# Kernel tuning notes

Measured on AMD Instinct MI355X. Metric: run time of the kernel, lower is better.

Reference implementation:

```python
import jax, jax.numpy as jnp
import numpy as np

MAX_DEG = 3
DEG_DIMS = [1, 3, 5, 7]          # degree_to_dim(d) = 2d+1
SUM_DIM = 16                     # sum of DEG_DIMS
FREQ_SUM = 44                    # sum over (d_in,d_out) of 2*min(d_in,d_out)+1
C = 32                           # channels per degree (in == out, FULL fusion)
EDGE_DIM = 2                     # fiber_edge[0] + 1
MID = 32                         # RadialProfile mid_dim
E = 4096
N = 1024


def setup_inputs() -> dict:
    key = jax.random.key(0)
    ks = jax.random.split(key, 16)
    inp = {}
    for d, dim in enumerate(DEG_DIMS):
        inp[f"node_feats_{d}"] = jax.random.normal(ks[d], (N, C, dim), jnp.float32)
    inp["edge_feats_0"] = jax.random.normal(ks[4], (E, EDGE_DIM, 1), jnp.float32)
    inp["basis"] = jax.random.normal(ks[5], (E, SUM_DIM, FREQ_SUM, SUM_DIM), jnp.float32)
    inp["src"] = jax.random.randint(ks[6], (E,), 0, N, dtype=jnp.int32)
    inp["dst"] = jax.random.randint(ks[7], (E,), 0, N, dtype=jnp.int32)
    # RadialProfile params: Linear(2,32) -> ReLU -> Linear(32,32) -> ReLU -> Linear(32, 44*32*32, bias=False)
    inp["w1"] = jax.random.normal(ks[8], (EDGE_DIM, MID), jnp.float32) / np.sqrt(EDGE_DIM)
    inp["b1"] = jnp.zeros((MID,), jnp.float32)
    inp["w2"] = jax.random.normal(ks[9], (MID, MID), jnp.float32) / np.sqrt(MID)
    inp["b2"] = jnp.zeros((MID,), jnp.float32)
    inp["w3"] = jax.random.normal(ks[10], (MID, FREQ_SUM * C * C), jnp.float32) / np.sqrt(MID)
    # self-interaction kernels per output degree
    for d in range(MAX_DEG + 1):
        inp[f"kernel_self_{d}"] = jax.random.normal(ks[11 + d], (C, C), jnp.float32) / np.sqrt(C)
    return inp


def _conv_se3(node_feats, edge_feats_0, basis, src, dst,
              w1, b1, w2, b2, w3, kernels_self):
    e = edge_feats_0.shape[0]
    # invariant edge feats: [E, edge_dim]
    inv = edge_feats_0[..., 0]
    # gather source node features and fuse along representation dim: [E, C, 16]
    feats = jnp.concatenate([nf[src] for nf in node_feats], axis=-1)
    # RadialProfile MLP -> radial weights [E, C_out, C_in * FREQ_SUM]
    h = jax.nn.relu(inv @ w1 + b1)
    h = jax.nn.relu(h @ w2 + b2)
    radial_weights = (h @ w3).reshape(e, C, C * FREQ_SUM)
    # VersatileConvSE3 fused path:
    # tmp = (features @ basis_view).view(E, C*FREQ_SUM, SUM_DIM)
    basis_view = basis.reshape(e, SUM_DIM, FREQ_SUM * SUM_DIM)
    tmp = jnp.einsum('eci,eix->ecx', feats, basis_view).reshape(e, C * FREQ_SUM, SUM_DIM)
    out_fused = jnp.einsum('eok,eks->eos', radial_weights, tmp)  # [E, C, 16]
    # unfuse by degree, add self-interaction at dst, pool (copy_e_sum) to nodes
    outs = []
    off = 0
    for d, dim in enumerate(DEG_DIMS):
        o = out_fused[..., off:off + dim]
        o = o + jnp.einsum('oc,ecd->eod', kernels_self[d], node_feats[d][dst])
        outs.append(jax.ops.segment_sum(o, dst, num_segments=N))
        off += dim
    # return fused node output [N, C, 16] (concat of degrees 0..3)
    return jnp.concatenate(outs, axis=-1)


def reference(node_feats_0, node_feats_1, node_feats_2, node_feats_3,
              edge_feats_0, basis, src, dst,
              w1, b1, w2, b2, w3,
              kernel_self_0, kernel_self_1, kernel_self_2, kernel_self_3):
    return _conv_se3([node_feats_0, node_feats_1, node_feats_2, node_feats_3],
                     edge_feats_0, basis, src, dst,
                     w1, b1, w2, b2, w3,
                     [kernel_self_0, kernel_self_1, kernel_self_2, kernel_self_3])
```

## Files before the change

kernel.cpp:

```cpp
#include <hip/hip_runtime.h>
#include <hip/hip_bf16.h>

#define NN 1024
#define EE 4096
#define CC 32
#define SD 16
#define FQ 44
#define MIDC 32
#define EB 16
#define NFQ 4
#define FPB 11

typedef short s16x4 __attribute__((ext_vector_type(4)));
typedef short s16x8 __attribute__((ext_vector_type(8)));
typedef float fx4 __attribute__((ext_vector_type(4)));

__device__ __forceinline__ unsigned short f2b(float x) {
    __hip_bfloat16 b = __float2bfloat16(x);
    return *reinterpret_cast<unsigned short*>(&b);
}

__device__ __forceinline__ s16x4 pack4(float a, float b, float c, float d) {
    s16x4 r;
    r[0] = (short)f2b(a); r[1] = (short)f2b(b);
    r[2] = (short)f2b(c); r[3] = (short)f2b(d);
    return r;
}

__device__ __forceinline__ fx4 mfma16(s16x4 a, s16x4 b, fx4 c) {
#if defined(__HIP_DEVICE_COMPILE__)
#if __has_builtin(__builtin_amdgcn_mfma_f32_16x16x16_bf16)
    return __builtin_amdgcn_mfma_f32_16x16x16_bf16(a, b, c, 0, 0, 0);
#else
    return __builtin_amdgcn_mfma_f32_16x16x16bf16_1k(a, b, c, 0, 0, 0);
#endif
#else
    return c;
#endif
}

__global__ __launch_bounds__(256) void k_w3t2(const float* __restrict__ w3,
                                              unsigned short* __restrict__ w3t2) {
    int tid = blockIdx.x * 256 + threadIdx.x;
    int m = tid & 31;
    int o = (tid >> 5) & 31;
    int c = tid >> 10;
    const float* rp = &w3[(size_t)m * 45056 + o * 1408 + c * 44];
    float v[44];
#pragma unroll
    for (int q = 0; q < 11; q++) {
        float4 t4 = *(const float4*)(rp + q * 4);
        v[q * 4 + 0] = t4.x; v[q * 4 + 1] = t4.y;
        v[q * 4 + 2] = t4.z; v[q * 4 + 3] = t4.w;
    }
#pragma unroll
    for (int f = 0; f < FQ; f++) {
        w3t2[(((size_t)f * CC + o) * CC + c) * CC + m] = f2b(v[f]);
    }
}

__global__ __launch_bounds__(256) void k_h(const float* __restrict__ ef,
                                           const float* __restrict__ w1,
                                           const float* __restrict__ b1,
                                           const float* __restrict__ w2,
                                           const float* __restrict__ b2,
                                           const int* __restrict__ dst,
                                           unsigned short* __restrict__ h2,
                                           int* __restrict__ deg) {
    int e = blockIdx.x * 256 + threadIdx.x;
    if (e >= EE) return;
    float i0 = ef[e * 2 + 0], i1 = ef[e * 2 + 1];
    float h1[MIDC];
#pragma unroll
    for (int j = 0; j < MIDC; j++) {
        float v = i0 * w1[j] + i1 * w1[MIDC + j] + b1[j];
        h1[j] = v > 0.f ? v : 0.f;
    }
    for (int j = 0; j < MIDC; j++) {
        float v = b2[j];
#pragma unroll
        for (int m = 0; m < MIDC; m++) v += h1[m] * w2[m * MIDC + j];
        v = v > 0.f ? v : 0.f;
        h2[e * MIDC + j] = f2b(v);
    }
    atomicAdd(&deg[dst[e]], 1);
}

__global__ __launch_bounds__(512, 4) void k_main(
    const float* __restrict__ nf0, const float* __restrict__ nf1,
    const float* __restrict__ nf2, const float* __restrict__ nf3,
    const float* __restrict__ basis, const int* __restrict__ src,
    const int* __restrict__ dst, const unsigned short* __restrict__ h2,
    const unsigned short* __restrict__ w3t2, float* __restrict__ out) {
    __shared__ __align__(16) unsigned short rad_lds[EB * CC * CC];

    int t = threadIdx.x;
    int wv = t >> 6;
    int l = t & 63;
    int l15 = l & 15;
    int kg = l >> 4;
    int eg = blockIdx.x >> 2;
    int fq = blockIdx.x & 3;
    int eb = eg * EB;
    int f0 = fq * FPB;

    s16x8 h2frag = *(const s16x8*)(h2 + ((size_t)(eb + l15) * MIDC + (kg << 3)));

    s16x4 fa[2][2];
#pragma unroll
    for (int ei = 0; ei < 2; ei++) {
        int sn = src[eb + (wv << 1) + ei];
#pragma unroll
        for (int ch = 0; ch < 2; ch++) {
            int c = (ch << 4) + l15;
            s16x4 v;
#pragma unroll
            for (int j = 0; j < 4; j++) {
                int i = (kg << 2) + j;
                float x;
                if (i < 1) x = nf0[sn * CC + c];
                else if (i < 4) x = nf1[(sn * CC + c) * 3 + (i - 1)];
                else if (i < 9) x = nf2[(sn * CC + c) * 5 + (i - 4)];
                else x = nf3[(sn * CC + c) * 7 + (i - 9)];
                v[j] = (short)f2b(x);
            }
            fa[ei][ch] = v;
        }
    }

    int radw[8];
#pragma unroll
    for (int j = 0; j < 8; j++) {
        int o = (wv << 2) + (j >> 1), ch = j & 1;
        int b = (l15 << 11) | (o << 6) | (ch << 5) | (kg << 3);
        radw[j] = b ^ (((l15 ^ o) & 15) << 3);
    }
    int rada[2][2][2];
#pragma unroll
    for (int ei = 0; ei < 2; ei++) {
        int e = (wv << 1) + ei;
#pragma unroll
        for (int oh = 0; oh < 2; oh++) {
            int o = (oh << 4) + l15;
#pragma unroll
            for (int ch = 0; ch < 2; ch++) {
                int b = (e << 11) | (o << 6) | (ch << 5) | (kg << 3);
                rada[ei][oh][ch] = b ^ (((e ^ o) & 15) << 3);
            }
        }
    }

    fx4 acc[2][2];
#pragma unroll
    for (int q = 0; q < 4; q++) acc[q >> 1][q & 1] = (fx4){0.f, 0.f, 0.f, 0.f};
    fx4 zz = (fx4){0.f, 0.f, 0.f, 0.f};

    s16x8 w[8];
    float pf[2][4];

#define LOAD_W(F)                                                                       \
    {                                                                                   \
        _Pragma("unroll") for (int j = 0; j < 8; j++) {                                 \
            int o_ = (wv << 2) + (j >> 1), ch_ = j & 1;                                 \
            w[j] = *(const s16x8*)(w3t2 +                                               \
                ((((size_t)(F) * CC + o_) * CC + (ch_ << 4) + l15) * CC + (kg << 3)));  \
        }                                                                               \
    }
#define LOAD_PF(F)                                                                      \
    {                                                                                   \
        _Pragma("unroll") for (int ei_ = 0; ei_ < 2; ei_++) {                           \
            const float* bp = basis +                                                   \
                (((size_t)(eb + (wv << 1) + ei_) * SD + (kg << 2)) * FQ + (F)) * SD +   \
                l15;                                                                    \
            _Pragma("unroll") for (int j = 0; j < 4; j++)                               \
                pf[ei_][j] = bp[(size_t)j * (FQ * SD)];                                 \
        }                                                                               \
    }

    LOAD_W(f0);
    LOAD_PF(f0);

    for (int fi = 0; fi < FPB; fi++) {
        __builtin_amdgcn_s_setprio(1);
#pragma unroll
        for (int j = 0; j < 8; j++) {
            fx4 cf = __builtin_amdgcn_mfma_f32_16x16x32_bf16(w[j], h2frag, zz, 0, 0, 0);
            *(s16x4*)((char*)rad_lds + radw[j]) = pack4(cf[0], cf[1], cf[2], cf[3]);
        }
        __builtin_amdgcn_s_setprio(0);
        s16x4 bbf[2];
#pragma unroll
        for (int ei = 0; ei < 2; ei++)
            bbf[ei] = pack4(pf[ei][0], pf[ei][1], pf[ei][2], pf[ei][3]);
        if (fi + 1 < FPB) {
            int fn = f0 + fi + 1;
            LOAD_W(fn);
            LOAD_PF(fn);
        }
        __syncthreads();

        __builtin_amdgcn_s_setprio(1);
#pragma unroll
        for (int ei = 0; ei < 2; ei++) {
#pragma unroll
            for (int ch = 0; ch < 2; ch++) {
                fx4 u = mfma16(fa[ei][ch], bbf[ei], zz);
                s16x4 ub = pack4(u[0], u[1], u[2], u[3]);
#pragma unroll
                for (int oh = 0; oh < 2; oh++) {
                    s16x4 ra = *(const s16x4*)((char*)rad_lds + rada[ei][oh][ch]);
                    acc[ei][oh] = mfma16(ra, ub, acc[ei][oh]);
                }
            }
        }
        __builtin_amdgcn_s_setprio(0);
        __syncthreads();
    }

#pragma unroll
    for (int ei = 0; ei < 2; ei++) {
        int e = (wv << 1) + ei;
        int d = dst[eb + e];
        float* op = &out[(size_t)d * (CC * SD)];
#pragma unroll
        for (int oh = 0; oh < 2; oh++) {
#pragma unroll
            for (int r = 0; r < 4; r++) {
                int o = (oh << 4) + (kg << 2) + r;
                atomicAdd(&op[o * SD + l15], acc[ei][oh][r]);
            }
        }
    }
}

__global__ __launch_bounds__(256) void k_self(
    const float* __restrict__ nf0, const float* __restrict__ nf1,
    const float* __restrict__ nf2, const float* __restrict__ nf3,
    const float* __restrict__ ks0, const float* __restrict__ ks1,
    const float* __restrict__ ks2, const float* __restrict__ ks3,
    const int* __restrict__ deg, float* __restrict__ out) {
    int idx = blockIdx.x * 256 + threadIdx.x;
    if (idx >= NN * CC * SD) return;
    int n = idx >> 9;
    int rem = idx & 511;
    int o = rem >> 4;
    int s = rem & 15;
    const float* nf;
    const float* ks;
    int dim, off;
    if (s < 1) { nf = nf0; ks = ks0; dim = 1; off = 0; }
    else if (s < 4) { nf = nf1; ks = ks1; dim = 3; off = 1; }
    else if (s < 9) { nf = nf2; ks = ks2; dim = 5; off = 4; }
    else { nf = nf3; ks = ks3; dim = 7; off = 9; }
    int j = s - off;
    float acc = 0.f;
#pragma unroll
    for (int c = 0; c < CC; c++) acc += ks[o * CC + c] * nf[(n * CC + c) * dim + j];
    out[idx] += (float)deg[n] * acc;
}

extern "C" void kernel_launch(void* const* d_in, const int* in_sizes, int n_in,
                              void* d_out, int out_size, void* d_ws, size_t ws_size,
                              hipStream_t stream) {
    const float* nf0 = (const float*)d_in[0];
    const float* nf1 = (const float*)d_in[1];
    const float* nf2 = (const float*)d_in[2];
    const float* nf3 = (const float*)d_in[3];
    const float* ef = (const float*)d_in[4];
    const float* basis = (const float*)d_in[5];
    const int* src = (const int*)d_in[6];
    const int* dst = (const int*)d_in[7];
    const float* w1 = (const float*)d_in[8];
    const float* b1 = (const float*)d_in[9];
    const float* w2 = (const float*)d_in[10];
    const float* b2 = (const float*)d_in[11];
    const float* w3 = (const float*)d_in[12];
    const float* ks0 = (const float*)d_in[13];
    const float* ks1 = (const float*)d_in[14];
    const float* ks2 = (const float*)d_in[15];
    const float* ks3 = (const float*)d_in[16];
    float* out = (float*)d_out;

    unsigned short* h2 = (unsigned short*)d_ws;
    int* deg = (int*)((char*)d_ws + EE * MIDC * 2);
    unsigned short* w3t2 = (unsigned short*)((char*)d_ws + EE * MIDC * 2 + 4096);

    (void)hipMemsetAsync(d_out, 0, (size_t)out_size * sizeof(float), stream);
    (void)hipMemsetAsync(deg, 0, NN * sizeof(int), stream);

    k_w3t2<<<128, 256, 0, stream>>>(w3, w3t2);
    k_h<<<EE / 256, 256, 0, stream>>>(ef, w1, b1, w2, b2, dst, h2, deg);
    k_main<<<(EE / EB) * NFQ, 512, 0, stream>>>(nf0, nf1, nf2, nf3, basis, src, dst,
                                                h2, w3t2, out);
    k_self<<<(NN * CC * SD) / 256, 256, 0, stream>>>(nf0, nf1, nf2, nf3, ks0, ks1,
                                                     ks2, ks3, deg, out);
}
```

Before: 125.5 us.

## Double-buffer radial weights in LDS to drop one barrier per frequency step

Radial weights go into two LDS buffers. Each step computes the next frequency's weights into the other buffer while consuming the current one, so only one __syncthreads per iteration remains instead of two. Basis prefetch is now two steps ahead through ping-pong register slots, and the loop is fully unrolled. This doubles LDS use per block (from 32 KB to 64 KB), which may reduce occupancy under the 512-thread, 4-blocks launch bounds, and it raises register pressure.

```diff
diff --git a/kernel.cpp b/kernel.cpp
--- a/kernel.cpp
+++ b/kernel.cpp
@@ -92,7 +92,7 @@
     const float* __restrict__ basis, const int* __restrict__ src,
     const int* __restrict__ dst, const unsigned short* __restrict__ h2,
     const unsigned short* __restrict__ w3t2, float* __restrict__ out) {
-    __shared__ __align__(16) unsigned short rad_lds[EB * CC * CC];
+    __shared__ __align__(16) unsigned short rad_lds[2][EB * CC * CC];
 
     int t = threadIdx.x;
     int wv = t >> 6;
@@ -156,7 +156,7 @@
     fx4 zz = (fx4){0.f, 0.f, 0.f, 0.f};
 
     s16x8 w[8];
-    float pf[2][4];
+    float pfA[2][4], pfB[2][4];
 
 #define LOAD_W(F)                                                                       \
     {                                                                                   \
@@ -166,38 +166,54 @@
                 ((((size_t)(F) * CC + o_) * CC + (ch_ << 4) + l15) * CC + (kg << 3)));  \
         }                                                                               \
     }
-#define LOAD_PF(F)                                                                      \
+#define LOAD_PF(F, SLOT)                                                                \
     {                                                                                   \
         _Pragma("unroll") for (int ei_ = 0; ei_ < 2; ei_++) {                           \
             const float* bp = basis +                                                   \
                 (((size_t)(eb + (wv << 1) + ei_) * SD + (kg << 2)) * FQ + (F)) * SD +   \
                 l15;                                                                    \
             _Pragma("unroll") for (int j = 0; j < 4; j++)                               \
-                pf[ei_][j] = bp[(size_t)j * (FQ * SD)];                                 \
+                SLOT[ei_][j] = bp[(size_t)j * (FQ * SD)];                               \
         }                                                                               \
     }
-
+#define RAD(BUF)                                                                        \
+    {                                                                                   \
+        __builtin_amdgcn_s_setprio(1);                                                  \
+        _Pragma("unroll") for (int j = 0; j < 8; j++) {                                 \
+            fx4 cf = __builtin_amdgcn_mfma_f32_16x16x32_bf16(w[j], h2frag, zz, 0, 0, 0);\
+            *(s16x4*)((char*)rad_lds[BUF] + radw[j]) = pack4(cf[0], cf[1], cf[2], cf[3]);\
+        }                                                                               \
+        __builtin_amdgcn_s_setprio(0);                                                  \
+    }
+
+    LOAD_PF(f0, pfA);
     LOAD_W(f0);
-    LOAD_PF(f0);
-
+    RAD(0);
+    s16x4 bbf[2];
+    bbf[0] = pack4(pfA[0][0], pfA[0][1], pfA[0][2], pfA[0][3]);
+    bbf[1] = pack4(pfA[1][0], pfA[1][1], pfA[1][2], pfA[1][3]);
+    LOAD_PF(f0 + 1, pfA);
+    LOAD_W(f0 + 1);
+    __syncthreads();
+
+#pragma unroll
     for (int fi = 0; fi < FPB; fi++) {
-        __builtin_amdgcn_s_setprio(1);
-#pragma unroll
-        for (int j = 0; j < 8; j++) {
-            fx4 cf = __builtin_amdgcn_mfma_f32_16x16x32_bf16(w[j], h2frag, zz, 0, 0, 0);
-            *(s16x4*)((char*)rad_lds + radw[j]) = pack4(cf[0], cf[1], cf[2], cf[3]);
-        }
-        __builtin_amdgcn_s_setprio(0);
-        s16x4 bbf[2];
-#pragma unroll
-        for (int ei = 0; ei < 2; ei++)
-            bbf[ei] = pack4(pf[ei][0], pf[ei][1], pf[ei][2], pf[ei][3]);
-        if (fi + 1 < FPB) {
-            int fn = f0 + fi + 1;
-            LOAD_W(fn);
-            LOAD_PF(fn);
-        }
-        __syncthreads();
+        int f = f0 + fi;
+        int cur = fi & 1;
+        if (fi + 2 < FPB) {
+            if (cur == 0) { LOAD_PF(f + 2, pfB); }
+            else          { LOAD_PF(f + 2, pfA); }
+        }
+        if (fi + 1 < FPB) RAD(cur ^ 1);
+        s16x4 bbf_next[2];
+        if (cur == 0) {
+            bbf_next[0] = pack4(pfA[0][0], pfA[0][1], pfA[0][2], pfA[0][3]);
+            bbf_next[1] = pack4(pfA[1][0], pfA[1][1], pfA[1][2], pfA[1][3]);
+        } else {
+            bbf_next[0] = pack4(pfB[0][0], pfB[0][1], pfB[0][2], pfB[0][3]);
+            bbf_next[1] = pack4(pfB[1][0], pfB[1][1], pfB[1][2], pfB[1][3]);
+        }
+        if (fi + 2 < FPB) LOAD_W(f + 2);
 
         __builtin_amdgcn_s_setprio(1);
 #pragma unroll
@@ -208,12 +224,14 @@
                 s16x4 ub = pack4(u[0], u[1], u[2], u[3]);
 #pragma unroll
                 for (int oh = 0; oh < 2; oh++) {
-                    s16x4 ra = *(const s16x4*)((char*)rad_lds + rada[ei][oh][ch]);
+                    s16x4 ra = *(const s16x4*)((char*)rad_lds[cur] + rada[ei][oh][ch]);
                     acc[ei][oh] = mfma16(ra, ub, acc[ei][oh]);
                 }
             }
         }
         __builtin_amdgcn_s_setprio(0);
+        bbf[0] = bbf_next[0];
+        bbf[1] = bbf_next[1];
         __syncthreads();
     }
 
```

New measurement: 122.4 us. 2.5% less time.

## Process 64 edges per block to reuse radial weights and restructure pipeline

Applied to the files above, without the earlier changes.

Each block now handles 64 edges instead of 16. Every loaded w3t2 fragment is multiplied against four h2 fragments, so global and L2 traffic for radial weights per edge falls. Basis prefetch is moved ahead of the radial MFMAs and the w3 prefetch after them. A custom waitcnt+barrier replaces __syncthreads, and the trailing barrier on the last iteration is skipped. The trade-off is a 128KB LDS buffer and much larger register arrays, which limit the kernel to one block per CU and sharply cut latency hiding. The grid also shrinks to 256 blocks.

```diff
diff --git a/kernel.cpp b/kernel.cpp
--- a/kernel.cpp
+++ b/kernel.cpp
@@ -7,7 +7,7 @@
 #define SD 16
 #define FQ 44
 #define MIDC 32
-#define EB 16
+#define EB 64
 #define NFQ 4
 #define FPB 11
 
@@ -38,6 +38,9 @@
     return c;
 #endif
 }
+
+#define CBAR() asm volatile("s_waitcnt lgkmcnt(0)\n\ts_barrier" ::: "memory")
+#define MEMFENCE() asm volatile("" ::: "memory")
 
 __global__ __launch_bounds__(256) void k_w3t2(const float* __restrict__ w3,
                                               unsigned short* __restrict__ w3t2) {
@@ -86,7 +89,7 @@
     atomicAdd(&deg[dst[e]], 1);
 }
 
-__global__ __launch_bounds__(512, 4) void k_main(
+__global__ __launch_bounds__(512, 2) void k_main(
     const float* __restrict__ nf0, const float* __restrict__ nf1,
     const float* __restrict__ nf2, const float* __restrict__ nf3,
     const float* __restrict__ basis, const int* __restrict__ src,
@@ -96,20 +99,22 @@
 
     int t = threadIdx.x;
     int wv = t >> 6;
-    int l = t & 63;
-    int l15 = l & 15;
-    int kg = l >> 4;
-    int eg = blockIdx.x >> 2;
-    int fq = blockIdx.x & 3;
+    int l15 = t & 15;
+    int kg = (t >> 4) & 3;
+    int fq = blockIdx.x >> 6;
+    int eg = blockIdx.x & 63;
     int eb = eg * EB;
     int f0 = fq * FPB;
 
-    s16x8 h2frag = *(const s16x8*)(h2 + ((size_t)(eb + l15) * MIDC + (kg << 3)));
-
-    s16x4 fa[2][2];
-#pragma unroll
-    for (int ei = 0; ei < 2; ei++) {
-        int sn = src[eb + (wv << 1) + ei];
+    s16x8 h2f[4];
+#pragma unroll
+    for (int es = 0; es < 4; es++)
+        h2f[es] = *(const s16x8*)(h2 + ((size_t)(eb + (es << 4) + l15) * MIDC + (kg << 3)));
+
+    s16x4 fa[8][2];
+#pragma unroll
+    for (int u = 0; u < 8; u++) {
+        int sn = src[eb + (wv << 3) + u];
 #pragma unroll
         for (int ch = 0; ch < 2; ch++) {
             int c = (ch << 4) + l15;
@@ -124,7 +129,7 @@
                 else x = nf3[(sn * CC + c) * 7 + (i - 9)];
                 v[j] = (short)f2b(x);
             }
-            fa[ei][ch] = v;
+            fa[u][ch] = v;
         }
     }
 
@@ -135,28 +140,20 @@
         int b = (l15 << 11) | (o << 6) | (ch << 5) | (kg << 3);
         radw[j] = b ^ (((l15 ^ o) & 15) << 3);
     }
-    int rada[2][2][2];
-#pragma unroll
-    for (int ei = 0; ei < 2; ei++) {
-        int e = (wv << 1) + ei;
-#pragma unroll
-        for (int oh = 0; oh < 2; oh++) {
-            int o = (oh << 4) + l15;
-#pragma unroll
-            for (int ch = 0; ch < 2; ch++) {
-                int b = (e << 11) | (o << 6) | (ch << 5) | (kg << 3);
-                rada[ei][oh][ch] = b ^ (((e ^ o) & 15) << 3);
-            }
-        }
-    }
-
-    fx4 acc[2][2];
-#pragma unroll
-    for (int q = 0; q < 4; q++) acc[q >> 1][q & 1] = (fx4){0.f, 0.f, 0.f, 0.f};
+    int rbase[8];
+#pragma unroll
+    for (int u = 0; u < 8; u++) {
+        int e = (wv << 3) + u;
+        rbase[u] = ((e << 11) | (l15 << 6) | (kg << 3)) ^ ((((e & 15) ^ l15) & 15) << 3);
+    }
+
+    fx4 acc[8][2];
+#pragma unroll
+    for (int q = 0; q < 16; q++) acc[q >> 1][q & 1] = (fx4){0.f, 0.f, 0.f, 0.f};
     fx4 zz = (fx4){0.f, 0.f, 0.f, 0.f};
 
     s16x8 w[8];
-    float pf[2][4];
+    float pf[8][4];
 
 #define LOAD_W(F)                                                                       \
     {                                                                                   \
@@ -165,69 +162,75 @@
             w[j] = *(const s16x8*)(w3t2 +                                               \
                 ((((size_t)(F) * CC + o_) * CC + (ch_ << 4) + l15) * CC + (kg << 3)));  \
         }                                                                               \
+        MEMFENCE();                                                                     \
     }
 #define LOAD_PF(F)                                                                      \
     {                                                                                   \
-        _Pragma("unroll") for (int ei_ = 0; ei_ < 2; ei_++) {                           \
+        _Pragma("unroll") for (int u_ = 0; u_ < 8; u_++) {                              \
             const float* bp = basis +                                                   \
-                (((size_t)(eb + (wv << 1) + ei_) * SD + (kg << 2)) * FQ + (F)) * SD +   \
+                (((size_t)(eb + (wv << 3) + u_) * SD + (kg << 2)) * FQ + (F)) * SD +    \
                 l15;                                                                    \
             _Pragma("unroll") for (int j = 0; j < 4; j++)                               \
-                pf[ei_][j] = bp[(size_t)j * (FQ * SD)];                                 \
+                pf[u_][j] = bp[(size_t)j * (FQ * SD)];                                  \
         }                                                                               \
-    }
-
+        MEMFENCE();                                                                     \
+    }
+
+    LOAD_PF(f0);
     LOAD_W(f0);
-    LOAD_PF(f0);
-
+
+#pragma unroll 1
     for (int fi = 0; fi < FPB; fi++) {
+        int f = f0 + fi;
+        s16x4 bbf[8];
+#pragma unroll
+        for (int u = 0; u < 8; u++)
+            bbf[u] = pack4(pf[u][0], pf[u][1], pf[u][2], pf[u][3]);
+        if (fi + 1 < FPB) LOAD_PF(f + 1);
+
         __builtin_amdgcn_s_setprio(1);
 #pragma unroll
         for (int j = 0; j < 8; j++) {
-            fx4 cf = __builtin_amdgcn_mfma_f32_16x16x32_bf16(w[j], h2frag, zz, 0, 0, 0);
-            *(s16x4*)((char*)rad_lds + radw[j]) = pack4(cf[0], cf[1], cf[2], cf[3]);
+#pragma unroll
+            for (int es = 0; es < 4; es++) {
+                fx4 cf = __builtin_amdgcn_mfma_f32_16x16x32_bf16(w[j], h2f[es], zz, 0, 0, 0);
+                *(s16x4*)((char*)rad_lds + radw[j] + (es << 15)) =
+                    pack4(cf[0], cf[1], cf[2], cf[3]);
+            }
         }
         __builtin_amdgcn_s_setprio(0);
-        s16x4 bbf[2];
-#pragma unroll
-        for (int ei = 0; ei < 2; ei++)
-            bbf[ei] = pack4(pf[ei][0], pf[ei][1], pf[ei][2], pf[ei][3]);
-        if (fi + 1 < FPB) {
-            int fn = f0 + fi + 1;
-            LOAD_W(fn);
-            LOAD_PF(fn);
-        }
-        __syncthreads();
+        if (fi + 1 < FPB) LOAD_W(f + 1);
+        CBAR();
 
         __builtin_amdgcn_s_setprio(1);
 #pragma unroll
-        for (int ei = 0; ei < 2; ei++) {
+        for (int u = 0; u < 8; u++) {
 #pragma unroll
             for (int ch = 0; ch < 2; ch++) {
-                fx4 u = mfma16(fa[ei][ch], bbf[ei], zz);
-                s16x4 ub = pack4(u[0], u[1], u[2], u[3]);
+                fx4 uu = mfma16(fa[u][ch], bbf[u], zz);
+                s16x4 ub = pack4(uu[0], uu[1], uu[2], uu[3]);
 #pragma unroll
                 for (int oh = 0; oh < 2; oh++) {
-                    s16x4 ra = *(const s16x4*)((char*)rad_lds + rada[ei][oh][ch]);
-                    acc[ei][oh] = mfma16(ra, ub, acc[ei][oh]);
+                    s16x4 ra = *(const s16x4*)((char*)rad_lds +
+                                               ((rbase[u] ^ (ch << 5)) + (oh << 10)));
+                    acc[u][oh] = mfma16(ra, ub, acc[u][oh]);
                 }
             }
         }
         __builtin_amdgcn_s_setprio(0);
-        __syncthreads();
-    }
-
-#pragma unroll
-    for (int ei = 0; ei < 2; ei++) {
-        int e = (wv << 1) + ei;
-        int d = dst[eb + e];
+        if (fi + 1 < FPB) CBAR();
+    }
+
+#pragma unroll
+    for (int u = 0; u < 8; u++) {
+        int d = dst[eb + (wv << 3) + u];
         float* op = &out[(size_t)d * (CC * SD)];
 #pragma unroll
         for (int oh = 0; oh < 2; oh++) {
 #pragma unroll
             for (int r = 0; r < 4; r++) {
                 int o = (oh << 4) + (kg << 2) + r;
-                atomicAdd(&op[o * SD + l15], acc[ei][oh][r]);
+                atomicAdd(&op[o * SD + l15], acc[u][oh][r]);
             }
         }
     }
```

After: 136.2 us. 8.5% more time.
